# Optimization experiments

Measured on AMD Instinct MI355X. Metric: run time of the kernel, lower is better.

The kernel has to match this reference:

```python
import jax, jax.numpy as jnp
import numpy as np

# Grid constants (must match fill_max of coordinate inputs)
B, T, Y, X = 2, 8, 128, 128
YO, XO = 2 * Y - 1, 2 * X - 1  # spconv transpose: (in-1)*2 - 2*1 + 3 = 2*in - 1
EPS = 1e-5


def setup_inputs() -> dict:
    key = jax.random.key(0)
    ks = jax.random.split(key, 8)
    N, CIN, COUT = 262144, 128, 64
    feats = jax.random.normal(ks[0], (N, CIN), dtype=jnp.float32)
    # kernel-offset-major weight layout [kt, ky, kx, Cin, Cout]
    weight = jax.random.normal(ks[1], (3, 3, 3, CIN, COUT), dtype=jnp.float32) * 0.05
    gamma = jnp.ones((COUT,), jnp.float32)
    beta = jnp.zeros((COUT,), jnp.float32)
    coords_b = jax.random.randint(ks[2], (N,), 0, B, dtype=jnp.int32)
    coords_t = jax.random.randint(ks[3], (N,), 0, T, dtype=jnp.int32)
    coords_y = jax.random.randint(ks[4], (N,), 0, Y, dtype=jnp.int32)
    coords_x = jax.random.randint(ks[5], (N,), 0, X, dtype=jnp.int32)
    return {"feats": feats, "weight": weight, "gamma": gamma, "beta": beta,
            "coords_b": coords_b, "coords_t": coords_t,
            "coords_y": coords_y, "coords_x": coords_x}


def _sparse_deconv(feats, weight, cb, ct, cy, cx):
    """Rulebook-style transpose conv: for each of 27 kernel offsets,
    GEMM the input features and scatter-add into the (dense) output grid.
    Output coord: out = in*stride - pad + k. Grid padded by 1 so out-of-range
    contributions land in the halo and are sliced away (equivalent to spconv
    dropping rules outside the output extent)."""
    COUT = weight.shape[-1]
    grid = jnp.zeros((B, T + 2, YO + 2, XO + 2, COUT), feats.dtype)
    cnt = jnp.zeros((B, T + 2, YO + 2, XO + 2), jnp.float32)
    ones = jnp.ones((feats.shape[0],), jnp.float32)
    for kt in range(3):
        ot = ct - 1 + kt + 1  # stride 1 in t; +1 = halo offset
        for ky in range(3):
            oy = 2 * cy - 1 + ky + 1
            for kx in range(3):
                ox = 2 * cx - 1 + kx + 1
                msg = feats @ weight[kt, ky, kx]  # [N, Cout]
                grid = grid.at[cb, ot, oy, ox].add(msg)
                cnt = cnt.at[cb, ot, oy, ox].add(ones)
    return grid[:, 1:-1, 1:-1, 1:-1], cnt[:, 1:-1, 1:-1, 1:-1]


def reference(feats, weight, gamma, beta, coords_b, coords_t, coords_y, coords_x):
    # sort_sparse_tensor only reorders voxels; math is order-invariant here.
    grid, cnt = _sparse_deconv(feats, weight, coords_b, coords_t, coords_y, coords_x)
    mask = (cnt > 0).astype(grid.dtype)  # active output sites [B,T,YO,XO]
    n = jnp.maximum(mask.sum(), 1.0)
    # BatchNorm1d over active-site features (grid is exactly 0 at inactive sites)
    mean = grid.sum(axis=(0, 1, 2, 3)) / n
    var = (grid * grid).sum(axis=(0, 1, 2, 3)) / n - mean * mean  # biased var
    rstd = jax.lax.rsqrt(var + EPS)
    out = (grid - mean) * (rstd * gamma) + beta
    out = out * mask[..., None]  # keep inactive sites at zero (sparse semantics)
    return jax.nn.relu(out)
```

## Files before the change

### kernel.cpp

```cpp
#include <hip/hip_runtime.h>
#include <hip/hip_bf16.h>

#define BB   2
#define TT   8
#define YY   128
#define XX   128
#define CINv 128
#define COUTv 64
#define YOv  255
#define XOv  255
#define NVOX 262144
#define NSITES (BB*TT*YY*XX)
#define CAP  16
#define OUT_SITES (BB*TT*YOv*XOv)
#define OUT_ELEMS ((size_t)OUT_SITES*COUTv)

typedef float  f32x4  __attribute__((ext_vector_type(4)));
typedef __bf16 bf16x8 __attribute__((ext_vector_type(8)));
typedef unsigned int u32x4 __attribute__((ext_vector_type(4)));

union FragU { u32x4 u; bf16x8 b; };
union Pack8 { unsigned short s[8]; u32x4 u; };

constexpr size_t OFF_STATS = 0;
constexpr size_t OFF_CNT   = 1024;
constexpr size_t ZERO_BYTES= OFF_CNT + 1048576;
constexpr size_t OFF_DBF   = ZERO_BYTES;
constexpr size_t OFF_PB    = OFF_DBF + 67108864;
constexpr size_t OFF_MASK  = OFF_PB + 442368;
constexpr size_t OFF_SS    = OFF_MASK + 1048576;
constexpr size_t OFF_IDX   = OFF_SS + 1024;
constexpr size_t OFF_OUTB  = OFF_IDX;

__device__ __forceinline__ unsigned short f2bf(float f) {
    unsigned u = __float_as_uint(f);
    u += 0x7fffu + ((u >> 16) & 1u);
    return (unsigned short)(u >> 16);
}

__device__ __forceinline__ void gld16(const void* g, void* l) {
    __builtin_amdgcn_global_load_lds(
        (const __attribute__((address_space(1))) unsigned int*)g,
        (__attribute__((address_space(3))) unsigned int*)l, 16, 0, 0);
}

__global__ __launch_bounds__(256) void k_count(
    const int* __restrict__ cb, const int* __restrict__ ct,
    const int* __restrict__ cy, const int* __restrict__ cx,
    unsigned int* __restrict__ cnt, int* __restrict__ idx)
{
    int n = blockIdx.x * 256 + threadIdx.x;
    int site = ((cb[n] * TT + ct[n]) * YY + cy[n]) * XX + cx[n];
    unsigned slot = atomicAdd(cnt + site, 1u);
    if (slot < CAP) idx[site * CAP + slot] = n;
}

__global__ __launch_bounds__(256) void k_gather(
    const float* __restrict__ feats,
    const unsigned int* __restrict__ cnt, const int* __restrict__ idx,
    unsigned short* __restrict__ Dbf)
{
    int tid = blockIdx.x * 256 + threadIdx.x;
    int site = tid >> 4;
    int c8 = (tid & 15) * 8;
    unsigned c = cnt[site]; if (c > CAP) c = CAP;
    float a[8] = {0.f,0.f,0.f,0.f,0.f,0.f,0.f,0.f};
    const int* ip = idx + (size_t)site * CAP;
    for (unsigned v = 0; v < c; ++v) {
        int n = ip[v];
        const float4 f0 = *(const float4*)(feats + (size_t)n * CINv + c8);
        const float4 f1 = *(const float4*)(feats + (size_t)n * CINv + c8 + 4);
        a[0] += f0.x; a[1] += f0.y; a[2] += f0.z; a[3] += f0.w;
        a[4] += f1.x; a[5] += f1.y; a[6] += f1.z; a[7] += f1.w;
    }
    Pack8 p;
    #pragma unroll
    for (int j = 0; j < 8; ++j) p.s[j] = f2bf(a[j]);
    *(u32x4*)(Dbf + (size_t)site * CINv + c8) = p.u;
}

__global__ __launch_bounds__(64) void k_pack(
    const float* __restrict__ W, unsigned short* __restrict__ PB)
{
    int f = blockIdx.x;
    int w  = f >> 4;
    int kc = (f >> 2) & 3;
    int nt = f & 3;
    int lane = threadIdx.x;
    int q = lane >> 4, col = lane & 15;
    Pack8 p;
    #pragma unroll
    for (int j = 0; j < 8; ++j) {
        int k  = kc * 32 + q * 8 + j;
        int nn = nt * 16 + col;
        p.s[j] = f2bf(W[((size_t)w * CINv + k) * COUTv + nn]);
    }
    *(u32x4*)(PB + ((size_t)f * 64 + lane) * 8) = p.u;
}

__global__ __launch_bounds__(256) void k_mask(
    const unsigned int* __restrict__ occ,
    unsigned char* __restrict__ mask, unsigned int* __restrict__ ncnt)
{
    int s = blockIdx.x * 256 + threadIdx.x;
    bool found = false;
    if (s < OUT_SITES) {
        int xo = s % XOv; int r = s / XOv;
        int yo = r % YOv; r /= YOv;
        int to = r & 7;   int b = r >> 3;
        int cts[3]; int ntc = 0;
        for (int kt = 0; kt < 3; ++kt) { int c = to + 1 - kt; if (c >= 0 && c < TT) cts[ntc++] = c; }
        int cys[2]; int nyc;
        if (yo & 1) { cys[0] = (yo + 1) >> 1; cys[1] = (yo - 1) >> 1; nyc = 2; }
        else        { cys[0] = yo >> 1; nyc = 1; }
        int cxs[2]; int nxc;
        if (xo & 1) { cxs[0] = (xo + 1) >> 1; cxs[1] = (xo - 1) >> 1; nxc = 2; }
        else        { cxs[0] = xo >> 1; nxc = 1; }
        for (int i = 0; i < ntc && !found; ++i)
            for (int j = 0; j < nyc && !found; ++j)
                for (int k = 0; k < nxc && !found; ++k)
                    if (occ[((b * TT + cts[i]) * YY + cys[j]) * XX + cxs[k]]) found = true;
        mask[s] = found ? 1 : 0;
    }
    unsigned long long bal = __ballot(found);
    if ((threadIdx.x & 63) == 0) {
        unsigned c = (unsigned)__popcll(bal);
        if (c) atomicAdd(ncnt, c);
    }
}


#define MFMA_BF16(A, B, C) __builtin_amdgcn_mfma_f32_16x16x32_bf16((A), (B), (C), 0, 0, 0)

#define BPASS2(bt, SLOT) do {                                                            \
    _Pragma("unroll")                                                                    \
    for (int kc = 0; kc < 4; ++kc) {                                                     \
        FragU Bf[4];                                                                     \
        _Pragma("unroll")                                                                \
        for (int nt = 0; nt < 4; ++nt)                                                   \
            Bf[nt].u = *(const u32x4*)((bt) + (size_t)((kc * 4 + nt) * 64 + lane) * 8);  \
        _Pragma("unroll")                                                                \
        for (int nt = 0; nt < 4; ++nt) {                                                 \
            acc0[SLOT][nt]     = MFMA_BF16(Aa0[kc].b, Bf[nt].b, acc0[SLOT][nt]);         \
            acc0[SLOT + 2][nt] = MFMA_BF16(Ab0[kc].b, Bf[nt].b, acc0[SLOT + 2][nt]);     \
            acc1[SLOT][nt]     = MFMA_BF16(Aa1[kc].b, Bf[nt].b, acc1[SLOT][nt]);         \
            acc1[SLOT + 2][nt] = MFMA_BF16(Ab1[kc].b, Bf[nt].b, acc1[SLOT + 2][nt]);     \
        }                                                                                \
    } } while (0)

__global__ __launch_bounds__(256, 2) void k_conv(
    const unsigned short* __restrict__ Dbf,
    const unsigned short* __restrict__ PB,
    unsigned short* __restrict__ outb,
    float* __restrict__ gsum, float* __restrict__ gsq)
{
    const int lane = threadIdx.x & 63;
    const int wave = threadIdx.x >> 6;
    const int bid = blockIdx.x;
    const int row_id = (bid & 7) * 256 + (bid >> 3);
    const int g  = row_id & 127;
    int r2 = row_id >> 7;
    const int to = r2 & 7;
    const int b  = r2 >> 3;

    int yo0; bool has2;
    if (g < 64)       { yo0 = 4 * g;            has2 = true;  }
    else if (g < 127) { yo0 = 4 * (g - 64) + 1; has2 = true;  }
    else              { yo0 = 253;              has2 = false; }

    const int m = lane & 15, q = lane >> 4;

    __shared__ __align__(16) unsigned short shB[3 * 16 * 64 * 8];
    __shared__ float shsum[64], shsq[64];
    if (threadIdx.x < 64) { shsum[threadIdx.x] = 0.f; shsq[threadIdx.x] = 0.f; }

    int ycy[2], yky[2], ny;
    if ((yo0 & 1) == 0) { ny = 1; ycy[0] = yo0 >> 1; yky[0] = 1; }
    else { ny = 2; ycy[0] = (yo0 + 1) >> 1; yky[0] = 0; ycy[1] = (yo0 - 1) >> 1; yky[1] = 2; }

    f32x4 acc0[4][4], acc1[4][4];
    #pragma unroll
    for (int ch = 0; ch < 4; ++ch)
        #pragma unroll
        for (int nt = 0; nt < 4; ++nt) {
            acc0[ch][nt] = (f32x4){0.f, 0.f, 0.f, 0.f};
            acc1[ch][nt] = (f32x4){0.f, 0.f, 0.f, 0.f};
        }

    for (int kt = 0; kt < 3; ++kt) {
        int ct = to + 1 - kt;
        if (ct < 0 || ct >= TT) continue;
        for (int iy = 0; iy < ny; ++iy) {
            __syncthreads();
            {
                const char* gsrc = (const char*)PB + (size_t)((kt * 3 + yky[iy]) * 3) * 16384;
                char* ldst = (char*)shB;
                #pragma unroll
                for (int r = 0; r < 12; ++r)
                    gld16(gsrc + r * 4096 + threadIdx.x * 16,
                          ldst + r * 4096 + wave * 1024);
            }
            int cy0 = ycy[iy];
            int cy1 = has2 ? cy0 + 1 : cy0;
            size_t plane0 = ((size_t)((b * TT + ct) * YY + cy0)) * XX;
            size_t plane1 = ((size_t)((b * TT + ct) * YY + cy1)) * XX;
            FragU Aa0[4], Ab0[4], Aa1[4], Ab1[4];
            {
                const unsigned short* pa0 = Dbf + (plane0 + (size_t)(2 * wave * 16 + m)) * CINv;
                const unsigned short* pb0 = Dbf + (plane0 + (size_t)((2 * wave + 1) * 16 + m)) * CINv;
                const unsigned short* pa1 = Dbf + (plane1 + (size_t)(2 * wave * 16 + m)) * CINv;
                const unsigned short* pb1 = Dbf + (plane1 + (size_t)((2 * wave + 1) * 16 + m)) * CINv;
                #pragma unroll
                for (int kc = 0; kc < 4; ++kc) {
                    Aa0[kc].u = *(const u32x4*)(pa0 + kc * 32 + q * 8);
                    Ab0[kc].u = *(const u32x4*)(pb0 + kc * 32 + q * 8);
                    Aa1[kc].u = *(const u32x4*)(pa1 + kc * 32 + q * 8);
                    Ab1[kc].u = *(const u32x4*)(pb1 + kc * 32 + q * 8);
                }
            }
            __syncthreads();

            BPASS2(shB + 8192,  0);
            BPASS2(shB + 16384, 1);

            {
                int cxb1 = (2 * wave + 1) * 16 + m + 1; if (cxb1 > 127) cxb1 = 127;
                const unsigned short* pa0 = Dbf + (plane0 + (size_t)(2 * wave * 16 + m + 1)) * CINv;
                const unsigned short* pb0 = Dbf + (plane0 + (size_t)cxb1) * CINv;
                const unsigned short* pa1 = Dbf + (plane1 + (size_t)(2 * wave * 16 + m + 1)) * CINv;
                const unsigned short* pb1 = Dbf + (plane1 + (size_t)cxb1) * CINv;
                #pragma unroll
                for (int kc = 0; kc < 4; ++kc) {
                    Aa0[kc].u = *(const u32x4*)(pa0 + kc * 32 + q * 8);
                    Ab0[kc].u = *(const u32x4*)(pb0 + kc * 32 + q * 8);
                    Aa1[kc].u = *(const u32x4*)(pa1 + kc * 32 + q * 8);
                    Ab1[kc].u = *(const u32x4*)(pb1 + kc * 32 + q * 8);
                }
            }
            BPASS2(shB + 0, 1);
        }
    }

    float sl[4] = {0.f,0.f,0.f,0.f}, sq[4] = {0.f,0.f,0.f,0.f};
    {
        size_t rowbase = ((size_t)((b * TT + to) * YOv + yo0)) * XOv;
        #pragma unroll
        for (int ch = 0; ch < 4; ++ch) {
            int cb8 = 2 * wave + (ch >> 1);
            int px = ch & 1;
            #pragma unroll
            for (int nt = 0; nt < 4; ++nt) {
                int c = nt * 16 + m;
                #pragma unroll
                for (int i = 0; i < 4; ++i) {
                    int r = q * 4 + i;
                    int xo = 2 * (cb8 * 16 + r) + px;
                    if (xo < XOv) {
                        float v = acc0[ch][nt][i];
                        outb[(rowbase + xo) * COUTv + c] = f2bf(v);
                        sl[nt] += v; sq[nt] += v * v;
                    }
                }
            }
        }
    }
    if (has2) {
        size_t rowbase = ((size_t)((b * TT + to) * YOv + (yo0 + 2))) * XOv;
        #pragma unroll
        for (int ch = 0; ch < 4; ++ch) {
            int cb8 = 2 * wave + (ch >> 1);
            int px = ch & 1;
            #pragma unroll
            for (int nt = 0; nt < 4; ++nt) {
                int c = nt * 16 + m;
                #pragma unroll
                for (int i = 0; i < 4; ++i) {
                    int r = q * 4 + i;
                    int xo = 2 * (cb8 * 16 + r) + px;
                    if (xo < XOv) {
                        float v = acc1[ch][nt][i];
                        outb[(rowbase + xo) * COUTv + c] = f2bf(v);
                        sl[nt] += v; sq[nt] += v * v;
                    }
                }
            }
        }
    }
    #pragma unroll
    for (int nt = 0; nt < 4; ++nt) {
        sl[nt] += __shfl_xor(sl[nt], 16); sl[nt] += __shfl_xor(sl[nt], 32);
        sq[nt] += __shfl_xor(sq[nt], 16); sq[nt] += __shfl_xor(sq[nt], 32);
    }
    if (lane < 16) {
        #pragma unroll
        for (int nt = 0; nt < 4; ++nt) {
            atomicAdd(&shsum[nt * 16 + lane], sl[nt]);
            atomicAdd(&shsq [nt * 16 + lane], sq[nt]);
        }
    }
    __syncthreads();
    if (threadIdx.x < 64) {
        unsafeAtomicAdd(&gsum[threadIdx.x], shsum[threadIdx.x]);
        unsafeAtomicAdd(&gsq [threadIdx.x], shsq [threadIdx.x]);
    }
}

__global__ __launch_bounds__(64) void k_final(
    const float* __restrict__ gsum, const float* __restrict__ gsq,
    const unsigned int* __restrict__ ncnt,
    const float* __restrict__ gamma, const float* __restrict__ beta,
    float* __restrict__ scale, float* __restrict__ shift)
{
    int c = threadIdx.x;
    float nf = (float)max(*ncnt, 1u);
    float mean = gsum[c] / nf;
    float var  = gsq[c] / nf - mean * mean;
    float rstd = rsqrtf(var + 1e-5f);
    float sc = rstd * gamma[c];
    scale[c] = sc;
    shift[c] = beta[c] - mean * sc;
}

__global__ __launch_bounds__(256) void k_norm(
    const unsigned short* __restrict__ outb, float* __restrict__ out,
    const unsigned char* __restrict__ mask,
    const float* __restrict__ scale, const float* __restrict__ shift)
{
    __shared__ float ssc[64], ssh[64];
    if (threadIdx.x < 64) { ssc[threadIdx.x] = scale[threadIdx.x]; ssh[threadIdx.x] = shift[threadIdx.x]; }
    __syncthreads();
    size_t t = (size_t)blockIdx.x * 256 + threadIdx.x;
    size_t e = t * 8;
    if (e >= OUT_ELEMS) return;
    Pack8 p; p.u = *(const u32x4*)(outb + e);
    int c = (int)(e & 63);
    size_t site = e >> 6;
    float4 v0, v1;
    if (mask[site]) {
        float w[8];
        #pragma unroll
        for (int j = 0; j < 8; ++j) {
            float f = __uint_as_float((unsigned)p.s[j] << 16);
            w[j] = fmaxf(fmaf(f, ssc[c + j], ssh[c + j]), 0.f);
        }
        v0 = make_float4(w[0], w[1], w[2], w[3]);
        v1 = make_float4(w[4], w[5], w[6], w[7]);
    } else {
        v0 = make_float4(0.f, 0.f, 0.f, 0.f);
        v1 = v0;
    }
    *(float4*)(out + e) = v0;
    *(float4*)(out + e + 4) = v1;
}

extern "C" void kernel_launch(void* const* d_in, const int* in_sizes, int n_in,
                              void* d_out, int out_size, void* d_ws, size_t ws_size,
                              hipStream_t stream)
{
    const float* feats = (const float*)d_in[0];
    const float* W     = (const float*)d_in[1];
    const float* gamma = (const float*)d_in[2];
    const float* beta  = (const float*)d_in[3];
    const int* cb = (const int*)d_in[4];
    const int* ct = (const int*)d_in[5];
    const int* cy = (const int*)d_in[6];
    const int* cx = (const int*)d_in[7];
    float* out = (float*)d_out;

    char* ws = (char*)d_ws;
    float*          gsum = (float*)(ws + OFF_STATS);
    float*          gsq  = gsum + 64;
    unsigned int*   ncnt = (unsigned int*)(ws + OFF_STATS + 512);
    unsigned int*   cnt  = (unsigned int*)(ws + OFF_CNT);
    unsigned short* Dbf  = (unsigned short*)(ws + OFF_DBF);
    unsigned short* PB   = (unsigned short*)(ws + OFF_PB);
    unsigned char*  mask = (unsigned char*)(ws + OFF_MASK);
    float*          scale= (float*)(ws + OFF_SS);
    float*          shift= scale + 64;
    int*            idx  = (int*)(ws + OFF_IDX);
    unsigned short* outb = (unsigned short*)(ws + OFF_OUTB);

    hipMemsetAsync(d_ws, 0, ZERO_BYTES, stream);

    k_count<<<NVOX / 256, 256, 0, stream>>>(cb, ct, cy, cx, cnt, idx);
    k_gather<<<NSITES * 16 / 256, 256, 0, stream>>>(feats, cnt, idx, Dbf);
    k_pack<<<27 * 16, 64, 0, stream>>>(W, PB);
    k_mask<<<(OUT_SITES + 255) / 256, 256, 0, stream>>>(cnt, mask, ncnt);
    k_conv<<<2048, 256, 0, stream>>>(Dbf, PB, outb, gsum, gsq);
    k_final<<<1, 64, 0, stream>>>(gsum, gsq, ncnt, gamma, beta, scale, shift);
    k_norm<<<(int)((OUT_ELEMS / 8 + 255) / 256), 256, 0, stream>>>(outb, out, mask, scale, shift);
}
```

Measured before the change: 826.5 us.

## Read packed weights directly from global memory in conv and batch gather index loads

The conv kernel no longer stages each weight tap into shared memory with global-to-LDS copies and block barriers. Each wave now reads its B fragments straight from global memory, relying on L1/L2 caching of the small packed weight buffer. This removes two barriers per (kt, iy) iteration and the 48 KB LDS footprint, which may allow more resident blocks. The trade-off is redundant global/L1 traffic, since all four waves fetch the same weights. Separately, the gather kernel loads the first four voxel indices with one int4 and unrolls their feature loads to raise memory-level parallelism.

New measurement: 933.1 us. 1.13x slower.

```diff
diff --git a/kernel.cpp b/kernel.cpp
--- a/kernel.cpp
+++ b/kernel.cpp
@@ -38,12 +38,6 @@
     return (unsigned short)(u >> 16);
 }
 
-__device__ __forceinline__ void gld16(const void* g, void* l) {
-    __builtin_amdgcn_global_load_lds(
-        (const __attribute__((address_space(1))) unsigned int*)g,
-        (__attribute__((address_space(3))) unsigned int*)l, 16, 0, 0);
-}
-
 __global__ __launch_bounds__(256) void k_count(
     const int* __restrict__ cb, const int* __restrict__ ct,
     const int* __restrict__ cy, const int* __restrict__ cx,
@@ -66,12 +60,26 @@
     unsigned c = cnt[site]; if (c > CAP) c = CAP;
     float a[8] = {0.f,0.f,0.f,0.f,0.f,0.f,0.f,0.f};
     const int* ip = idx + (size_t)site * CAP;
-    for (unsigned v = 0; v < c; ++v) {
-        int n = ip[v];
-        const float4 f0 = *(const float4*)(feats + (size_t)n * CINv + c8);
-        const float4 f1 = *(const float4*)(feats + (size_t)n * CINv + c8 + 4);
-        a[0] += f0.x; a[1] += f0.y; a[2] += f0.z; a[3] += f0.w;
-        a[4] += f1.x; a[5] += f1.y; a[6] += f1.z; a[7] += f1.w;
+    if (c) {
+        const int4 i4 = *(const int4*)ip;
+        int nv[4] = { i4.x, i4.y, i4.z, i4.w };
+        #pragma unroll
+        for (int v = 0; v < 4; ++v) {
+            if ((unsigned)v < c) {
+                int n = nv[v];
+                const float4 f0 = *(const float4*)(feats + (size_t)n * CINv + c8);
+                const float4 f1 = *(const float4*)(feats + (size_t)n * CINv + c8 + 4);
+                a[0] += f0.x; a[1] += f0.y; a[2] += f0.z; a[3] += f0.w;
+                a[4] += f1.x; a[5] += f1.y; a[6] += f1.z; a[7] += f1.w;
+            }
+        }
+        for (unsigned v = 4; v < c; ++v) {
+            int n = ip[v];
+            const float4 f0 = *(const float4*)(feats + (size_t)n * CINv + c8);
+            const float4 f1 = *(const float4*)(feats + (size_t)n * CINv + c8 + 4);
+            a[0] += f0.x; a[1] += f0.y; a[2] += f0.z; a[3] += f0.w;
+            a[4] += f1.x; a[5] += f1.y; a[6] += f1.z; a[7] += f1.w;
+        }
     }
     Pack8 p;
     #pragma unroll
@@ -132,13 +140,14 @@
 
 #define MFMA_BF16(A, B, C) __builtin_amdgcn_mfma_f32_16x16x32_bf16((A), (B), (C), 0, 0, 0)
 
-#define BPASS2(bt, SLOT) do {                                                            \
+#define BPASS2G(wtap, SLOT) do {                                                         \
+    const unsigned short* bt = PB + (size_t)(wtap) * (16 * 64 * 8);                      \
     _Pragma("unroll")                                                                    \
     for (int kc = 0; kc < 4; ++kc) {                                                     \
         FragU Bf[4];                                                                     \
         _Pragma("unroll")                                                                \
         for (int nt = 0; nt < 4; ++nt)                                                   \
-            Bf[nt].u = *(const u32x4*)((bt) + (size_t)((kc * 4 + nt) * 64 + lane) * 8);  \
+            Bf[nt].u = *(const u32x4*)(bt + (size_t)((kc * 4 + nt) * 64 + lane) * 8);    \
         _Pragma("unroll")                                                                \
         for (int nt = 0; nt < 4; ++nt) {                                                 \
             acc0[SLOT][nt]     = MFMA_BF16(Aa0[kc].b, Bf[nt].b, acc0[SLOT][nt]);         \
@@ -170,7 +179,6 @@
 
     const int m = lane & 15, q = lane >> 4;
 
-    __shared__ __align__(16) unsigned short shB[3 * 16 * 64 * 8];
     __shared__ float shsum[64], shsq[64];
     if (threadIdx.x < 64) { shsum[threadIdx.x] = 0.f; shsq[threadIdx.x] = 0.f; }
 
@@ -191,19 +199,12 @@
         int ct = to + 1 - kt;
         if (ct < 0 || ct >= TT) continue;
         for (int iy = 0; iy < ny; ++iy) {
-            __syncthreads();
-            {
-                const char* gsrc = (const char*)PB + (size_t)((kt * 3 + yky[iy]) * 3) * 16384;
-                char* ldst = (char*)shB;
-                #pragma unroll
-                for (int r = 0; r < 12; ++r)
-                    gld16(gsrc + r * 4096 + threadIdx.x * 16,
-                          ldst + r * 4096 + wave * 1024);
-            }
             int cy0 = ycy[iy];
             int cy1 = has2 ? cy0 + 1 : cy0;
             size_t plane0 = ((size_t)((b * TT + ct) * YY + cy0)) * XX;
             size_t plane1 = ((size_t)((b * TT + ct) * YY + cy1)) * XX;
+            const int wbase = (kt * 3 + yky[iy]) * 3;
+
             FragU Aa0[4], Ab0[4], Aa1[4], Ab1[4];
             {
                 const unsigned short* pa0 = Dbf + (plane0 + (size_t)(2 * wave * 16 + m)) * CINv;
@@ -218,10 +219,9 @@
                     Ab1[kc].u = *(const u32x4*)(pb1 + kc * 32 + q * 8);
                 }
             }
-            __syncthreads();
-
-            BPASS2(shB + 8192,  0);
-            BPASS2(shB + 16384, 1);
+
+            BPASS2G(wbase + 1, 0);
+            BPASS2G(wbase + 2, 1);
 
             {
                 int cxb1 = (2 * wave + 1) * 16 + m + 1; if (cxb1 > 127) cxb1 = 127;
@@ -237,7 +237,7 @@
                     Ab1[kc].u = *(const u32x4*)(pb1 + kc * 32 + q * 8);
                 }
             }
-            BPASS2(shB + 0, 1);
+            BPASS2G(wbase + 0, 1);
         }
     }
 
@@ -291,6 +291,7 @@
         sl[nt] += __shfl_xor(sl[nt], 16); sl[nt] += __shfl_xor(sl[nt], 32);
         sq[nt] += __shfl_xor(sq[nt], 16); sq[nt] += __shfl_xor(sq[nt], 32);
     }
+    __syncthreads();
     if (lane < 16) {
         #pragma unroll
         for (int nt = 0; nt < 4; ++nt) {
```

## Double conv block size to share B tile across two output row pairs; vectorize gather index load

Applied to the files above, without the earlier changes.

k_conv now runs 512-thread blocks in which two groups of four waves each compute a different pair of output rows. Both groups share one LDS copy of the packed weight slices, which halves the global-to-LDS weight traffic per output row. The gather kernel loads the first four voxel indices with a single int4 read and unrolls their feature loads, so independent memory requests can be in flight together. The change raises register and occupancy pressure through the new launch bounds and reworks the row mapping, including the edge row at 253/254.

Measured after the change: 1.738 ms. 2.1x slower.

```diff
diff --git a/kernel.cpp b/kernel.cpp
--- a/kernel.cpp
+++ b/kernel.cpp
@@ -66,12 +66,26 @@
     unsigned c = cnt[site]; if (c > CAP) c = CAP;
     float a[8] = {0.f,0.f,0.f,0.f,0.f,0.f,0.f,0.f};
     const int* ip = idx + (size_t)site * CAP;
-    for (unsigned v = 0; v < c; ++v) {
-        int n = ip[v];
-        const float4 f0 = *(const float4*)(feats + (size_t)n * CINv + c8);
-        const float4 f1 = *(const float4*)(feats + (size_t)n * CINv + c8 + 4);
-        a[0] += f0.x; a[1] += f0.y; a[2] += f0.z; a[3] += f0.w;
-        a[4] += f1.x; a[5] += f1.y; a[6] += f1.z; a[7] += f1.w;
+    if (c) {
+        const int4 i4 = *(const int4*)ip;
+        int nv[4] = { i4.x, i4.y, i4.z, i4.w };
+        #pragma unroll
+        for (int v = 0; v < 4; ++v) {
+            if ((unsigned)v < c) {
+                int n = nv[v];
+                const float4 f0 = *(const float4*)(feats + (size_t)n * CINv + c8);
+                const float4 f1 = *(const float4*)(feats + (size_t)n * CINv + c8 + 4);
+                a[0] += f0.x; a[1] += f0.y; a[2] += f0.z; a[3] += f0.w;
+                a[4] += f1.x; a[5] += f1.y; a[6] += f1.z; a[7] += f1.w;
+            }
+        }
+        for (unsigned v = 4; v < c; ++v) {
+            int n = ip[v];
+            const float4 f0 = *(const float4*)(feats + (size_t)n * CINv + c8);
+            const float4 f1 = *(const float4*)(feats + (size_t)n * CINv + c8 + 4);
+            a[0] += f0.x; a[1] += f0.y; a[2] += f0.z; a[3] += f0.w;
+            a[4] += f1.x; a[5] += f1.y; a[6] += f1.z; a[7] += f1.w;
+        }
     }
     Pack8 p;
     #pragma unroll
@@ -148,7 +162,7 @@
         }                                                                                \
     } } while (0)
 
-__global__ __launch_bounds__(256, 2) void k_conv(
+__global__ __launch_bounds__(512, 4) void k_conv(
     const unsigned short* __restrict__ Dbf,
     const unsigned short* __restrict__ PB,
     unsigned short* __restrict__ outb,
@@ -156,17 +170,19 @@
 {
     const int lane = threadIdx.x & 63;
     const int wave = threadIdx.x >> 6;
-    const int bid = blockIdx.x;
-    const int row_id = (bid & 7) * 256 + (bid >> 3);
-    const int g  = row_id & 127;
-    int r2 = row_id >> 7;
+    const int w2   = wave & 3;
+    const int p    = wave >> 2;
+    const int bid  = blockIdx.x;
+    const int row_id = (bid & 7) * 128 + (bid >> 3);
+    const int g  = row_id & 63;
+    int r2 = row_id >> 6;
     const int to = r2 & 7;
     const int b  = r2 >> 3;
 
-    int yo0; bool has2;
-    if (g < 64)       { yo0 = 4 * g;            has2 = true;  }
-    else if (g < 127) { yo0 = 4 * (g - 64) + 1; has2 = true;  }
-    else              { yo0 = 253;              has2 = false; }
+    const int yo0 = (g < 32) ? (8 * g) : (8 * (g - 32) + 1);
+    const int yoA = yo0 + 4 * p;
+    const int yoB = yoA + 2;
+    const bool has2 = (yoB <= 254);
 
     const int m = lane & 15, q = lane >> 4;
 
@@ -196,20 +212,20 @@
                 const char* gsrc = (const char*)PB + (size_t)((kt * 3 + yky[iy]) * 3) * 16384;
                 char* ldst = (char*)shB;
                 #pragma unroll
-                for (int r = 0; r < 12; ++r)
-                    gld16(gsrc + r * 4096 + threadIdx.x * 16,
-                          ldst + r * 4096 + wave * 1024);
-            }
-            int cy0 = ycy[iy];
-            int cy1 = has2 ? cy0 + 1 : cy0;
-            size_t plane0 = ((size_t)((b * TT + ct) * YY + cy0)) * XX;
-            size_t plane1 = ((size_t)((b * TT + ct) * YY + cy1)) * XX;
+                for (int r = 0; r < 6; ++r)
+                    gld16(gsrc + r * 8192 + threadIdx.x * 16,
+                          ldst + r * 8192 + wave * 1024);
+            }
+            int cyA = ycy[iy] + 2 * p;
+            int cyB = has2 ? cyA + 1 : cyA;
+            size_t plane0 = ((size_t)((b * TT + ct) * YY + cyA)) * XX;
+            size_t plane1 = ((size_t)((b * TT + ct) * YY + cyB)) * XX;
             FragU Aa0[4], Ab0[4], Aa1[4], Ab1[4];
             {
-                const unsigned short* pa0 = Dbf + (plane0 + (size_t)(2 * wave * 16 + m)) * CINv;
-                const unsigned short* pb0 = Dbf + (plane0 + (size_t)((2 * wave + 1) * 16 + m)) * CINv;
-                const unsigned short* pa1 = Dbf + (plane1 + (size_t)(2 * wave * 16 + m)) * CINv;
-                const unsigned short* pb1 = Dbf + (plane1 + (size_t)((2 * wave + 1) * 16 + m)) * CINv;
+                const unsigned short* pa0 = Dbf + (plane0 + (size_t)(2 * w2 * 16 + m)) * CINv;
+                const unsigned short* pb0 = Dbf + (plane0 + (size_t)((2 * w2 + 1) * 16 + m)) * CINv;
+                const unsigned short* pa1 = Dbf + (plane1 + (size_t)(2 * w2 * 16 + m)) * CINv;
+                const unsigned short* pb1 = Dbf + (plane1 + (size_t)((2 * w2 + 1) * 16 + m)) * CINv;
                 #pragma unroll
                 for (int kc = 0; kc < 4; ++kc) {
                     Aa0[kc].u = *(const u32x4*)(pa0 + kc * 32 + q * 8);
@@ -224,10 +240,10 @@
             BPASS2(shB + 16384, 1);
 
             {
-                int cxb1 = (2 * wave + 1) * 16 + m + 1; if (cxb1 > 127) cxb1 = 127;
-                const unsigned short* pa0 = Dbf + (plane0 + (size_t)(2 * wave * 16 + m + 1)) * CINv;
+                int cxb1 = (2 * w2 + 1) * 16 + m + 1; if (cxb1 > 127) cxb1 = 127;
+                const unsigned short* pa0 = Dbf + (plane0 + (size_t)(2 * w2 * 16 + m + 1)) * CINv;
                 const unsigned short* pb0 = Dbf + (plane0 + (size_t)cxb1) * CINv;
-                const unsigned short* pa1 = Dbf + (plane1 + (size_t)(2 * wave * 16 + m + 1)) * CINv;
+                const unsigned short* pa1 = Dbf + (plane1 + (size_t)(2 * w2 * 16 + m + 1)) * CINv;
                 const unsigned short* pb1 = Dbf + (plane1 + (size_t)cxb1) * CINv;
                 #pragma unroll
                 for (int kc = 0; kc < 4; ++kc) {
@@ -243,10 +259,10 @@
 
     float sl[4] = {0.f,0.f,0.f,0.f}, sq[4] = {0.f,0.f,0.f,0.f};
     {
-        size_t rowbase = ((size_t)((b * TT + to) * YOv + yo0)) * XOv;
+        size_t rowbase = ((size_t)((b * TT + to) * YOv + yoA)) * XOv;
         #pragma unroll
         for (int ch = 0; ch < 4; ++ch) {
-            int cb8 = 2 * wave + (ch >> 1);
+            int cb8 = 2 * w2 + (ch >> 1);
             int px = ch & 1;
             #pragma unroll
             for (int nt = 0; nt < 4; ++nt) {
@@ -265,10 +281,10 @@
         }
     }
     if (has2) {
-        size_t rowbase = ((size_t)((b * TT + to) * YOv + (yo0 + 2))) * XOv;
+        size_t rowbase = ((size_t)((b * TT + to) * YOv + yoB)) * XOv;
         #pragma unroll
         for (int ch = 0; ch < 4; ++ch) {
-            int cb8 = 2 * wave + (ch >> 1);
+            int cb8 = 2 * w2 + (ch >> 1);
             int px = ch & 1;
             #pragma unroll
             for (int nt = 0; nt < 4; ++nt) {
@@ -386,7 +402,7 @@
     k_gather<<<NSITES * 16 / 256, 256, 0, stream>>>(feats, cnt, idx, Dbf);
     k_pack<<<27 * 16, 64, 0, stream>>>(W, PB);
     k_mask<<<(OUT_SITES + 255) / 256, 256, 0, stream>>>(cnt, mask, ncnt);
-    k_conv<<<2048, 256, 0, stream>>>(Dbf, PB, outb, gsum, gsq);
+    k_conv<<<1024, 512, 0, stream>>>(Dbf, PB, outb, gsum, gsq);
     k_final<<<1, 64, 0, stream>>>(gsum, gsq, ncnt, gamma, beta, scale, shift);
     k_norm<<<(int)((OUT_ELEMS / 8 + 255) / 256), 256, 0, stream>>>(outb, out, mask, scale, shift);
 }
```
